# Optimization experiments

Measured on AMD Instinct MI355X. Metric: run time of the kernel, lower is better.

Reference implementation:

```python
import jax, jax.numpy as jnp
import numpy as np

B, N, DIM = 16, 577, 768
HEADS, HEAD_DIM = 12, 64
QKV_DIM = HEADS * HEAD_DIM
MAX_REL = 14
TABLE_ROWS = 2 * MAX_REL + 2  # 30


def _rel_indices(n, max_rel):
    # Static (shape-only) 2D relative-position index matrices with CLS padding.
    m = n - 1
    side = int(m ** 0.5)
    r = np.arange(m)
    dv = r[None, :] // side - r[:, None] // side
    dh = r[None, :] % side - r[:, None] % side
    iv = np.clip(dv, -max_rel, max_rel) + max_rel + 1
    ih = np.clip(dh, -max_rel, max_rel) + max_rel + 1
    iv = np.pad(iv, ((1, 0), (1, 0)))  # CLS row/col -> index 0
    ih = np.pad(ih, ((1, 0), (1, 0)))
    return jnp.asarray(iv), jnp.asarray(ih)


def setup_inputs() -> dict:
    key = jax.random.key(0)
    ks = jax.random.split(key, 8)
    return {
        "x": jax.random.normal(ks[0], (B, N, DIM), jnp.float32),
        "qkv_w": jax.random.normal(ks[1], (3 * QKV_DIM, DIM), jnp.float32) * 0.02,
        "proj_w": jax.random.normal(ks[2], (DIM, QKV_DIM), jnp.float32) * 0.02,
        "proj_b": jnp.zeros((DIM,), jnp.float32),
        "tab_kv": jax.random.normal(ks[3], (TABLE_ROWS, HEAD_DIM), jnp.float32) * 0.02,
        "tab_kh": jax.random.normal(ks[4], (TABLE_ROWS, HEAD_DIM), jnp.float32) * 0.02,
        "tab_vv": jax.random.normal(ks[5], (TABLE_ROWS, HEAD_DIM), jnp.float32) * 0.02,
        "tab_vh": jax.random.normal(ks[6], (TABLE_ROWS, HEAD_DIM), jnp.float32) * 0.02,
    }


def reference(x, qkv_w, proj_w, proj_b, tab_kv, tab_kh, tab_vv, tab_vh):
    b, n, _ = x.shape
    scale = HEAD_DIM ** -0.5
    # qkv: [b,n,3*qkv_dim] -> [3,b,h,n,d]
    qkv = (x @ qkv_w.T).reshape(b, n, 3, HEADS, HEAD_DIM).transpose(2, 0, 3, 1, 4)
    q, k, v = qkv[0], qkv[1], qkv[2]
    attn = jnp.einsum('bhqd,bhkd->bhqk', q, k) * scale
    iv, ih = _rel_indices(n, MAX_REL)
    r_p_k = tab_kv[iv] + tab_kh[ih]  # [n,n,d]
    attn = attn + jnp.einsum('bhqd,qkd->bhqk', q, r_p_k) * scale
    attn = jax.nn.softmax(attn, axis=-1)
    out = jnp.einsum('bhqk,bhkd->bhqd', attn, v)
    r_p_v = tab_vv[iv] + tab_vh[ih]  # [n,n,d]
    out = out + jnp.einsum('bhqk,qkd->bhqd', attn, r_p_v)
    out = out.transpose(0, 2, 1, 3).reshape(b, n, QKV_DIM)
    return out @ proj_w.T + proj_b
```

## Files before the change

kernel.cpp:

```cpp
#include <hip/hip_runtime.h>


#define BB    16
#define NNq   577
#define DIMM  768
#define NHh   12
#define HD    64
#define MM    9232
#define QT    64
#define KT    64
#define NPAD  640
#define NW3   2304

typedef _Float16 h8 __attribute__((ext_vector_type(8)));
typedef _Float16 h4 __attribute__((ext_vector_type(4)));
typedef float    f4 __attribute__((ext_vector_type(4)));

__device__ inline h8 pack8(float4 a, float4 b) {
    h8 r;
    r[0]=(_Float16)a.x; r[1]=(_Float16)a.y; r[2]=(_Float16)a.z; r[3]=(_Float16)a.w;
    r[4]=(_Float16)b.x; r[5]=(_Float16)b.y; r[6]=(_Float16)b.z; r[7]=(_Float16)b.w;
    return r;
}

__global__ void init_all(const float* __restrict__ x, const float* __restrict__ w,
                         const float* __restrict__ pw,
                         _Float16* __restrict__ M2g, _Float16* __restrict__ vh,
                         _Float16* __restrict__ xh, _Float16* __restrict__ wh,
                         _Float16* __restrict__ pwh)
{
    const size_t id = (size_t)blockIdx.x*256 + threadIdx.x;
    if (id < NPAD*64) {
        const int key = (int)id >> 6, bin = (int)id & 63;
        int vb = 255, hb = 255;
        if (key == 0)      { vb = 24; hb = 49; }
        else if (key < NNq){ const int kq = key-1, kv = kq/24; vb = kv; hb = 25 + (kq - kv*24); }
        M2g[bin*NPAD + key] =
            ((key < NNq) && (bin==vb || bin==hb || bin==50)) ? (_Float16)1.f : (_Float16)0.f;
        return;
    }
    const size_t vid = id - NPAD*64;
    if (vid < (size_t)BB*NHh*HD*64) {
        const int head = (int)(vid >> 12);
        const int rem  = (int)vid & 4095;
        const int d    = rem >> 6;
        const int col  = 576 + (rem & 63);
        vh[(size_t)head*(HD*NPAD) + (size_t)d*NPAD + col] = (_Float16)0.f;
        return;
    }
    const size_t cid = vid - (size_t)BB*NHh*HD*64;
    const size_t NX = (size_t)MM*DIMM/4;
    const size_t NW = (size_t)NW3*DIMM/4;
    const size_t NP = (size_t)DIMM*DIMM/4;
    const float4* src; h4* dst; size_t j;
    if (cid < NX)            { src = (const float4*)x;  dst = (h4*)xh;  j = cid; }
    else if (cid < NX+NW)    { src = (const float4*)w;  dst = (h4*)wh;  j = cid - NX; }
    else if (cid < NX+NW+NP) { src = (const float4*)pw; dst = (h4*)pwh; j = cid - NX - NW; }
    else return;
    const float4 v = src[j];
    h4 hh; hh[0]=(_Float16)v.x; hh[1]=(_Float16)v.y; hh[2]=(_Float16)v.z; hh[3]=(_Float16)v.w;
    dst[j] = hh;
}

template <typename F>
__device__ __forceinline__ void gemm128f2(const _Float16* __restrict__ Ah_g,
                                          const _Float16* __restrict__ Bh_g,
                                          F epi)
{
    __shared__ _Float16 Ah[128][72], Bh[128][72];
    const int t  = threadIdx.x;
    const int wv = t >> 6, lane = t & 63, lo = lane & 15, g = lane >> 4;
    const int gb = g << 3;
    const int wm = (wv >> 1) << 6, wn = (wv & 1) << 6;
    const int bm = blockIdx.y << 7, bn = blockIdx.x << 7;
    f4 acc[4][4] = {};
    const int lr = t >> 1;
    const int lc = (t & 1) << 5;
    const int am = bm + lr;
    const bool aok = am < MM;
    const _Float16* arh = Ah_g + (size_t)(aok ? am : 0) * DIMM + lc;
    const _Float16* brh = Bh_g + (size_t)(bn + lr) * DIMM + lc;

    for (int k0 = 0; k0 < DIMM; k0 += 64) {
        h8 a0 = {}, a1 = {}, a2 = {}, a3 = {};
        if (aok) {
            a0 = *(const h8*)(arh + k0);      a1 = *(const h8*)(arh + k0 + 8);
            a2 = *(const h8*)(arh + k0 + 16); a3 = *(const h8*)(arh + k0 + 24);
        }
        const h8 b0 = *(const h8*)(brh + k0),      b1 = *(const h8*)(brh + k0 + 8);
        const h8 b2 = *(const h8*)(brh + k0 + 16), b3 = *(const h8*)(brh + k0 + 24);
        __syncthreads();
        *(h8*)&Ah[lr][lc]    = a0; *(h8*)&Ah[lr][lc+8]  = a1;
        *(h8*)&Ah[lr][lc+16] = a2; *(h8*)&Ah[lr][lc+24] = a3;
        *(h8*)&Bh[lr][lc]    = b0; *(h8*)&Bh[lr][lc+8]  = b1;
        *(h8*)&Bh[lr][lc+16] = b2; *(h8*)&Bh[lr][lc+24] = b3;
        __syncthreads();
        {
            h8 fah[4], fbh[4];
            #pragma unroll
            for (int i = 0; i < 4; ++i) {
                fah[i] = *(const h8*)&Ah[wm + 16*i + lo][gb];
                fbh[i] = *(const h8*)&Bh[wn + 16*i + lo][gb];
            }
            #pragma unroll
            for (int mi = 0; mi < 4; ++mi) {
                #pragma unroll
                for (int ni = 0; ni < 4; ++ni)
                    acc[mi][ni] = __builtin_amdgcn_mfma_f32_16x16x32_f16(fah[mi], fbh[ni], acc[mi][ni], 0, 0, 0);
            }
        }
        {
            h8 fah[4], fbh[4];
            #pragma unroll
            for (int i = 0; i < 4; ++i) {
                fah[i] = *(const h8*)&Ah[wm + 16*i + lo][32 + gb];
                fbh[i] = *(const h8*)&Bh[wn + 16*i + lo][32 + gb];
            }
            #pragma unroll
            for (int mi = 0; mi < 4; ++mi) {
                #pragma unroll
                for (int ni = 0; ni < 4; ++ni)
                    acc[mi][ni] = __builtin_amdgcn_mfma_f32_16x16x32_f16(fah[mi], fbh[ni], acc[mi][ni], 0, 0, 0);
            }
        }
    }
    epi(acc, bm, bn, wm, wn, lo, g);
}

__global__ __launch_bounds__(256, 3)
void qkv_gemm(const _Float16* __restrict__ xh, const _Float16* __restrict__ wh,
              _Float16* __restrict__ qh, _Float16* __restrict__ kh, _Float16* __restrict__ vh)
{
    gemm128f2(xh, wh, [=](f4 (&acc)[4][4], int bm, int bn, int wm, int wn, int lo, int g) {
        const int three = bn / 768;
        const int cb    = bn - three * 768;
        #pragma unroll
        for (int mi = 0; mi < 4; ++mi) {
            #pragma unroll
            for (int reg = 0; reg < 4; ++reg) {
                const int m = bm + wm + 16*mi + 4*g + reg;
                if (m >= MM) continue;
                const int b_ = m / NNq;
                const int n_ = m - b_ * NNq;
                #pragma unroll
                for (int ni = 0; ni < 4; ++ni) {
                    const int n  = cb + wn + 16*ni + lo;
                    const int hh = n >> 6;
                    const int d  = n & 63;
                    if (three == 0) {
                        qh[((size_t)(b_*NHh + hh)*NPAD + n_)*HD + d] =
                            (_Float16)(acc[mi][ni][reg] * 0.18033688f);
                    } else if (three == 1) {
                        kh[((size_t)(b_*NHh + hh)*NPAD + n_)*HD + d] = (_Float16)acc[mi][ni][reg];
                    } else {
                        vh[((size_t)(b_*NHh + hh)*HD + d)*NPAD + n_] = (_Float16)acc[mi][ni][reg];
                    }
                }
            }
        }
    });
}

__global__ __launch_bounds__(256, 3)
void proj_gemm(const _Float16* __restrict__ aoh, const _Float16* __restrict__ pwh,
               const float* __restrict__ bias, float* __restrict__ out)
{
    gemm128f2(aoh, pwh, [=](f4 (&acc)[4][4], int bm, int bn, int wm, int wn, int lo, int g) {
        #pragma unroll
        for (int ni = 0; ni < 4; ++ni) {
            const int n  = bn + wn + 16*ni + lo;
            const float bb = bias[n];
            #pragma unroll
            for (int mi = 0; mi < 4; ++mi) {
                #pragma unroll
                for (int reg = 0; reg < 4; ++reg) {
                    const int m = bm + wm + 16*mi + 4*g + reg;
                    if (m >= MM) continue;
                    out[(size_t)m*DIMM + n] = acc[mi][ni][reg] + bb;
                }
            }
        }
    });
}

__global__ __launch_bounds__(256, 2)
void attn_fused(const _Float16* __restrict__ qh,
                const _Float16* __restrict__ kh, const _Float16* __restrict__ vh,
                const float* __restrict__ tkv, const float* __restrict__ tkh,
                const float* __restrict__ tvv, const float* __restrict__ tvh,
                const _Float16* __restrict__ M2g,
                _Float16* __restrict__ aoh)
{
    __shared__ __align__(16) char smem[34048];
    _Float16 (*qrelS)[72] = (_Float16(*)[72])(smem);
    _Float16 (*Pt)[72]    = (_Float16(*)[72])(smem + 9216);
    float    (*TvS)[65]   = (float(*)[65])(smem + 18432);
    float    (*binsS)[52] = (float(*)[52])(smem);

    const int t    = threadIdx.x;
    const int w    = t >> 6;
    const int lane = t & 63;
    const int lo   = lane & 15;
    const int g    = lane >> 4;
    const int gb   = g << 3;

    const int blk = blockIdx.x;
    const int x8  = blk & 7;
    const int r_  = blk >> 3;
    const int hq  = r_ / 10;
    const int qt  = r_ - hq*10;
    const int bh  = x8 + (hq << 3);
    const int qt0 = qt * QT;
    const int qrow = 16*w + 4*g;
    const _Float16* qp = qh + (size_t)bh * (NPAD*HD);
    const _Float16* kp = kh + (size_t)bh * (NPAD*HD);
    const _Float16* vp = vh + (size_t)bh * (HD*NPAD);

    for (int e = t; e < 60*64; e += 256) {
        const int r = e >> 6, d = e & 63;
        TvS[r][d] = (r < 30) ? tvv[r*HD + d] : tvh[(r-30)*HD + d];
    }

    const h8 a0 = *(const h8*)(qp + (size_t)(qt0 + 16*w + lo)*HD + gb);
    const h8 a1 = *(const h8*)(qp + (size_t)(qt0 + 16*w + lo)*HD + 32 + gb);

    {
        f4 qacc[4] = {f4{0,0,0,0}, f4{0,0,0,0}, f4{0,0,0,0}, f4{0,0,0,0}};
        #pragma unroll
        for (int c = 0; c < 4; ++c) {
            const int r16 = 16*c + lo;
            const float* src = (r16 < 30) ? (tkv + r16*HD) : (tkh + (r16-30)*HD);
            h8 tb0 = {}, tb1 = {};
            if (r16 < 60) {
                tb0 = pack8(*(const float4*)(src + gb),      *(const float4*)(src + gb + 4));
                tb1 = pack8(*(const float4*)(src + 32 + gb), *(const float4*)(src + 32 + gb + 4));
            }
            qacc[c] = __builtin_amdgcn_mfma_f32_16x16x32_f16(a0, tb0, qacc[c], 0, 0, 0);
            qacc[c] = __builtin_amdgcn_mfma_f32_16x16x32_f16(a1, tb1, qacc[c], 0, 0, 0);
        }
        #pragma unroll
        for (int c = 0; c < 4; ++c) {
            #pragma unroll
            for (int i = 0; i < 4; ++i)
                qrelS[qrow + i][16*c + lo] = (_Float16)qacc[c][i];
        }
    }

    int qv_[4], qh_[4];
    bool q0_[4];
    #pragma unroll
    for (int i = 0; i < 4; ++i) {
        const int qgl = qt0 + qrow + i;
        q0_[i] = (qgl == 0);
        int qq = qgl - 1; if (qq < 0) qq = 0;
        qv_[i] = qq / 24;
        qh_[i] = qq - qv_[i]*24;
    }

    f4 o_acc [4] = {f4{0,0,0,0}, f4{0,0,0,0}, f4{0,0,0,0}, f4{0,0,0,0}};
    f4 binacc[4] = {f4{0,0,0,0}, f4{0,0,0,0}, f4{0,0,0,0}, f4{0,0,0,0}};

    for (int kt0 = 0; kt0 < 576; kt0 += KT) {
        h8 kb0[4], kb1[4], v0r[4], v1r[4], m20[4], m21[4];
        #pragma unroll
        for (int c = 0; c < 4; ++c) {
            const int key = kt0 + 16*c + lo;
            kb0[c] = *(const h8*)(kp + (size_t)key*HD + gb);
            kb1[c] = *(const h8*)(kp + (size_t)key*HD + 32 + gb);
            const int dd = 16*c + lo;
            v0r[c] = *(const h8*)(vp + (size_t)dd*NPAD + kt0 + gb);
            v1r[c] = *(const h8*)(vp + (size_t)dd*NPAD + kt0 + 32 + gb);
            m20[c] = *(const h8*)(M2g + (size_t)dd*NPAD + kt0 + gb);
            m21[c] = *(const h8*)(M2g + (size_t)dd*NPAD + kt0 + 32 + gb);
        }
        float srel[4][4];
        #pragma unroll
        for (int c = 0; c < 4; ++c) {
            const int key = kt0 + 16*c + lo;
            int kk = key - 1; if (kk < 0) kk = 0;
            const int kv  = kk / 24;
            const int kh2 = kk - kv*24;
            const bool kz = (key == 0);
            #pragma unroll
            for (int i = 0; i < 4; ++i) {
                int colv, colh;
                if (kz || q0_[i]) { colv = 0; colh = 30; }
                else {
                    int dv = kv  - qv_[i]; dv = min(14, max(-14, dv));
                    int dh = kh2 - qh_[i]; dh = min(14, max(-14, dh));
                    colv = dv + 15;
                    colh = 45 + dh;
                }
                srel[c][i] = (float)qrelS[qrow+i][colv] + (float)qrelS[qrow+i][colh];
            }
        }
        f4 Sc[4];
        #pragma unroll
        for (int c = 0; c < 4; ++c) {
            f4 acc = f4{0,0,0,0};
            acc = __builtin_amdgcn_mfma_f32_16x16x32_f16(a0, kb0[c], acc, 0, 0, 0);
            acc = __builtin_amdgcn_mfma_f32_16x16x32_f16(a1, kb1[c], acc, 0, 0, 0);
            Sc[c] = acc;
        }
        #pragma unroll
        for (int c = 0; c < 4; ++c) {
            #pragma unroll
            for (int i = 0; i < 4; ++i) {
                const float p = exp2f(Sc[c][i] + srel[c][i]);
                Pt[qrow+i][16*c + lo] = (_Float16)p;
            }
        }
        const h8 p0 = *(const h8*)&Pt[16*w + lo][gb];
        const h8 p1 = *(const h8*)&Pt[16*w + lo][32 + gb];
        #pragma unroll
        for (int c = 0; c < 4; ++c) {
            binacc[c] = __builtin_amdgcn_mfma_f32_16x16x32_f16(p0, m20[c], binacc[c], 0, 0, 0);
            binacc[c] = __builtin_amdgcn_mfma_f32_16x16x32_f16(p1, m21[c], binacc[c], 0, 0, 0);
        }
        #pragma unroll
        for (int c = 0; c < 4; ++c) {
            o_acc[c] = __builtin_amdgcn_mfma_f32_16x16x32_f16(p0, v0r[c], o_acc[c], 0, 0, 0);
            o_acc[c] = __builtin_amdgcn_mfma_f32_16x16x32_f16(p1, v1r[c], o_acc[c], 0, 0, 0);
        }
    }

    {
        const int kt0 = 576;
        h8 kb0_, kb1_, v0r[4], v1r[4], m20[4], m21[4];
        kb0_ = *(const h8*)(kp + (size_t)(kt0 + lo)*HD + gb);
        kb1_ = *(const h8*)(kp + (size_t)(kt0 + lo)*HD + 32 + gb);
        #pragma unroll
        for (int c = 0; c < 4; ++c) {
            const int dd = 16*c + lo;
            v0r[c] = *(const h8*)(vp + (size_t)dd*NPAD + kt0 + gb);
            v1r[c] = *(const h8*)(vp + (size_t)dd*NPAD + kt0 + 32 + gb);
            m20[c] = *(const h8*)(M2g + (size_t)dd*NPAD + kt0 + gb);
            m21[c] = *(const h8*)(M2g + (size_t)dd*NPAD + kt0 + 32 + gb);
        }
        float srel0[4];
        {
            const int key = kt0 + lo;
            int kk = key - 1; if (kk < 0) kk = 0;
            const int kv  = kk / 24;
            const int kh2 = kk - kv*24;
            #pragma unroll
            for (int i = 0; i < 4; ++i) {
                int colv, colh;
                if (q0_[i]) { colv = 0; colh = 30; }
                else {
                    int dv = kv  - qv_[i]; dv = min(14, max(-14, dv));
                    int dh = kh2 - qh_[i]; dh = min(14, max(-14, dh));
                    colv = dv + 15;
                    colh = 45 + dh;
                }
                srel0[i] = (float)qrelS[qrow+i][colv] + (float)qrelS[qrow+i][colh];
            }
        }
        f4 Sc0 = f4{0,0,0,0};
        Sc0 = __builtin_amdgcn_mfma_f32_16x16x32_f16(a0, kb0_, Sc0, 0, 0, 0);
        Sc0 = __builtin_amdgcn_mfma_f32_16x16x32_f16(a1, kb1_, Sc0, 0, 0, 0);
        {
            const bool ok = (kt0 + lo) < NNq;
            #pragma unroll
            for (int i = 0; i < 4; ++i) {
                const float p = ok ? exp2f(Sc0[i] + srel0[i]) : 0.f;
                Pt[qrow+i][lo] = (_Float16)p;
            }
            #pragma unroll
            for (int c = 1; c < 4; ++c) {
                #pragma unroll
                for (int i = 0; i < 4; ++i)
                    Pt[qrow+i][16*c + lo] = (_Float16)0.f;
            }
        }
        const h8 p0 = *(const h8*)&Pt[16*w + lo][gb];
        const h8 p1 = *(const h8*)&Pt[16*w + lo][32 + gb];
        #pragma unroll
        for (int c = 0; c < 4; ++c) {
            binacc[c] = __builtin_amdgcn_mfma_f32_16x16x32_f16(p0, m20[c], binacc[c], 0, 0, 0);
            binacc[c] = __builtin_amdgcn_mfma_f32_16x16x32_f16(p1, m21[c], binacc[c], 0, 0, 0);
        }
        #pragma unroll
        for (int c = 0; c < 4; ++c) {
            o_acc[c] = __builtin_amdgcn_mfma_f32_16x16x32_f16(p0, v0r[c], o_acc[c], 0, 0, 0);
            o_acc[c] = __builtin_amdgcn_mfma_f32_16x16x32_f16(p1, v1r[c], o_acc[c], 0, 0, 0);
        }
    }

    __syncthreads();
    #pragma unroll
    for (int c = 0; c < 4; ++c) {
        const int bc = 16*c + lo;
        if (bc <= 50) {
            #pragma unroll
            for (int i = 0; i < 4; ++i) binsS[qrow+i][bc] = binacc[c][i];
        }
    }
    __syncthreads();

    const int b_ = bh / NHh;
    const int h_ = bh - b_*NHh;
    #pragma unroll
    for (int i = 0; i < 4; ++i) {
        const int qr  = qrow + i;
        const int qgl = qt0 + qr;
        if (qgl >= NNq) continue;
        const float l    = binsS[qr][50];
        const float invl = 1.f / l;
        float o[4] = {o_acc[0][i], o_acc[1][i], o_acc[2][i], o_acc[3][i]};
        if (qgl == 0) {
            #pragma unroll
            for (int c = 0; c < 4; ++c) {
                const int d = 16*c + lo;
                o[c] += l * (TvS[0][d] + TvS[30][d]);
            }
        } else {
            #pragma unroll
            for (int bin = 0; bin < 24; ++bin) {
                const float wq = binsS[qr][bin];
                int dv = bin - qv_[i]; dv = min(14, max(-14, dv));
                #pragma unroll
                for (int c = 0; c < 4; ++c) o[c] += wq * TvS[dv+15][16*c + lo];
            }
            {
                const float wq = binsS[qr][24];
                #pragma unroll
                for (int c = 0; c < 4; ++c) o[c] += wq * TvS[0][16*c + lo];
            }
            #pragma unroll
            for (int bin = 0; bin < 24; ++bin) {
                const float wq = binsS[qr][25+bin];
                int dh = bin - qh_[i]; dh = min(14, max(-14, dh));
                #pragma unroll
                for (int c = 0; c < 4; ++c) o[c] += wq * TvS[45+dh][16*c + lo];
            }
            {
                const float wq = binsS[qr][49];
                #pragma unroll
                for (int c = 0; c < 4; ++c) o[c] += wq * TvS[30][16*c + lo];
            }
        }
        _Float16* dst = aoh + (size_t)(b_*NNq + qgl)*DIMM + h_*HD;
        #pragma unroll
        for (int c = 0; c < 4; ++c) dst[16*c + lo] = (_Float16)(o[c] * invl);
    }
}

extern "C" void kernel_launch(void* const* d_in, const int* in_sizes, int n_in,
                              void* d_out, int out_size, void* d_ws, size_t ws_size,
                              hipStream_t stream)
{
    const float* x      = (const float*)d_in[0];
    const float* qkv_w  = (const float*)d_in[1];
    const float* proj_w = (const float*)d_in[2];
    const float* proj_b = (const float*)d_in[3];
    const float* tkv    = (const float*)d_in[4];
    const float* tkh    = (const float*)d_in[5];
    const float* tvv    = (const float*)d_in[6];
    const float* tvh    = (const float*)d_in[7];
    float* out = (float*)d_out;
    float* ws  = (float*)d_ws;

    const size_t KV = (size_t)BB * NHh * NPAD * HD;
    _Float16* qh  = (_Float16*)ws;
    _Float16* kh  = qh + KV;
    _Float16* vh  = kh + KV;
    _Float16* aoh = vh + KV;
    _Float16* M2g = aoh + (size_t)MM*DIMM;
    _Float16* xh  = M2g + NPAD*64;
    _Float16* wh  = xh + (size_t)MM*DIMM;
    _Float16* pwh = wh + (size_t)NW3*DIMM;

    dim3 b256(256, 1, 1);
    init_all<<<12460, b256, 0, stream>>>(x, qkv_w, proj_w, M2g, vh, xh, wh, pwh);

    dim3 g1(NW3/128, (MM + 127)/128, 1);
    qkv_gemm<<<g1, b256, 0, stream>>>(xh, wh, qh, kh, vh);

    attn_fused<<<dim3(1920,1,1), b256, 0, stream>>>(qh, kh, vh, tkv, tkh, tvv, tvh, M2g, aoh);

    dim3 g3(DIMM/128, (MM + 127)/128, 1);
    proj_gemm<<<g3, b256, 0, stream>>>(aoh, pwh, proj_b, out);
}
```

Before: 433.0 us.

## Process two 64-row query tiles per attention block to reuse K/V/M2 loads

Each attention workgroup now handles 128 query rows as two 64-row sub-tiles, so every K, V and M2 fragment loaded from global memory feeds twice the MFMA work. The grid is halved to 960 blocks and shared memory grows to hold the doubled qrel, P and bins buffers. The cost is more accumulator registers and LDS per block, which may lower occupancy under the 2-blocks-per-SIMD launch bound. The last tile also computes rows past 577 that are then discarded.

```diff
diff --git a/kernel.cpp b/kernel.cpp
--- a/kernel.cpp
+++ b/kernel.cpp
@@ -7,7 +7,6 @@
 #define NHh   12
 #define HD    64
 #define MM    9232
-#define QT    64
 #define KT    64
 #define NPAD  640
 #define NW3   2304
@@ -191,10 +190,10 @@
                 const _Float16* __restrict__ M2g,
                 _Float16* __restrict__ aoh)
 {
-    __shared__ __align__(16) char smem[34048];
+    __shared__ __align__(16) char smem[52464];
     _Float16 (*qrelS)[72] = (_Float16(*)[72])(smem);
-    _Float16 (*Pt)[72]    = (_Float16(*)[72])(smem + 9216);
-    float    (*TvS)[65]   = (float(*)[65])(smem + 18432);
+    _Float16 (*Pt)[72]    = (_Float16(*)[72])(smem + 18432);
+    float    (*TvS)[65]   = (float(*)[65])(smem + 36864);
     float    (*binsS)[52] = (float(*)[52])(smem);
 
     const int t    = threadIdx.x;
@@ -207,10 +206,10 @@
     const int blk = blockIdx.x;
     const int x8  = blk & 7;
     const int r_  = blk >> 3;
-    const int hq  = r_ / 10;
-    const int qt  = r_ - hq*10;
+    const int hq  = r_ / 5;
+    const int qt  = r_ - hq*5;
     const int bh  = x8 + (hq << 3);
-    const int qt0 = qt * QT;
+    const int qt0 = qt * 128;
     const int qrow = 16*w + 4*g;
     const _Float16* qp = qh + (size_t)bh * (NPAD*HD);
     const _Float16* kp = kh + (size_t)bh * (NPAD*HD);
@@ -221,11 +220,14 @@
         TvS[r][d] = (r < 30) ? tvv[r*HD + d] : tvh[(r-30)*HD + d];
     }
 
-    const h8 a0 = *(const h8*)(qp + (size_t)(qt0 + 16*w + lo)*HD + gb);
-    const h8 a1 = *(const h8*)(qp + (size_t)(qt0 + 16*w + lo)*HD + 32 + gb);
+    const h8 a0A = *(const h8*)(qp + (size_t)(qt0 +      16*w + lo)*HD + gb);
+    const h8 a1A = *(const h8*)(qp + (size_t)(qt0 +      16*w + lo)*HD + 32 + gb);
+    const h8 a0B = *(const h8*)(qp + (size_t)(qt0 + 64 + 16*w + lo)*HD + gb);
+    const h8 a1B = *(const h8*)(qp + (size_t)(qt0 + 64 + 16*w + lo)*HD + 32 + gb);
 
     {
-        f4 qacc[4] = {f4{0,0,0,0}, f4{0,0,0,0}, f4{0,0,0,0}, f4{0,0,0,0}};
+        f4 qaccA[4] = {f4{0,0,0,0}, f4{0,0,0,0}, f4{0,0,0,0}, f4{0,0,0,0}};
+        f4 qaccB[4] = {f4{0,0,0,0}, f4{0,0,0,0}, f4{0,0,0,0}, f4{0,0,0,0}};
         #pragma unroll
         for (int c = 0; c < 4; ++c) {
             const int r16 = 16*c + lo;
@@ -235,30 +237,39 @@
                 tb0 = pack8(*(const float4*)(src + gb),      *(const float4*)(src + gb + 4));
                 tb1 = pack8(*(const float4*)(src + 32 + gb), *(const float4*)(src + 32 + gb + 4));
             }
-            qacc[c] = __builtin_amdgcn_mfma_f32_16x16x32_f16(a0, tb0, qacc[c], 0, 0, 0);
-            qacc[c] = __builtin_amdgcn_mfma_f32_16x16x32_f16(a1, tb1, qacc[c], 0, 0, 0);
-        }
-        #pragma unroll
-        for (int c = 0; c < 4; ++c) {
-            #pragma unroll
-            for (int i = 0; i < 4; ++i)
-                qrelS[qrow + i][16*c + lo] = (_Float16)qacc[c][i];
-        }
-    }
-
-    int qv_[4], qh_[4];
-    bool q0_[4];
+            qaccA[c] = __builtin_amdgcn_mfma_f32_16x16x32_f16(a0A, tb0, qaccA[c], 0, 0, 0);
+            qaccA[c] = __builtin_amdgcn_mfma_f32_16x16x32_f16(a1A, tb1, qaccA[c], 0, 0, 0);
+            qaccB[c] = __builtin_amdgcn_mfma_f32_16x16x32_f16(a0B, tb0, qaccB[c], 0, 0, 0);
+            qaccB[c] = __builtin_amdgcn_mfma_f32_16x16x32_f16(a1B, tb1, qaccB[c], 0, 0, 0);
+        }
+        #pragma unroll
+        for (int c = 0; c < 4; ++c) {
+            #pragma unroll
+            for (int i = 0; i < 4; ++i) {
+                qrelS[qrow + i][16*c + lo]      = (_Float16)qaccA[c][i];
+                qrelS[64 + qrow + i][16*c + lo] = (_Float16)qaccB[c][i];
+            }
+        }
+    }
+
+    int qv_[2][4], qh_[2][4];
+    bool q0_[2][4];
     #pragma unroll
-    for (int i = 0; i < 4; ++i) {
-        const int qgl = qt0 + qrow + i;
-        q0_[i] = (qgl == 0);
-        int qq = qgl - 1; if (qq < 0) qq = 0;
-        qv_[i] = qq / 24;
-        qh_[i] = qq - qv_[i]*24;
-    }
-
-    f4 o_acc [4] = {f4{0,0,0,0}, f4{0,0,0,0}, f4{0,0,0,0}, f4{0,0,0,0}};
-    f4 binacc[4] = {f4{0,0,0,0}, f4{0,0,0,0}, f4{0,0,0,0}, f4{0,0,0,0}};
+    for (int tb = 0; tb < 2; ++tb) {
+        #pragma unroll
+        for (int i = 0; i < 4; ++i) {
+            const int qgl = qt0 + 64*tb + qrow + i;
+            q0_[tb][i] = (qgl == 0);
+            int qq = qgl - 1; if (qq < 0) qq = 0;
+            qv_[tb][i] = qq / 24;
+            qh_[tb][i] = qq - qv_[tb][i]*24;
+        }
+    }
+
+    f4 o_accA [4] = {f4{0,0,0,0}, f4{0,0,0,0}, f4{0,0,0,0}, f4{0,0,0,0}};
+    f4 binaccA[4] = {f4{0,0,0,0}, f4{0,0,0,0}, f4{0,0,0,0}, f4{0,0,0,0}};
+    f4 o_accB [4] = {f4{0,0,0,0}, f4{0,0,0,0}, f4{0,0,0,0}, f4{0,0,0,0}};
+    f4 binaccB[4] = {f4{0,0,0,0}, f4{0,0,0,0}, f4{0,0,0,0}, f4{0,0,0,0}};
 
     for (int kt0 = 0; kt0 < 576; kt0 += KT) {
         h8 kb0[4], kb1[4], v0r[4], v1r[4], m20[4], m21[4];
@@ -273,54 +284,95 @@
             m20[c] = *(const h8*)(M2g + (size_t)dd*NPAD + kt0 + gb);
             m21[c] = *(const h8*)(M2g + (size_t)dd*NPAD + kt0 + 32 + gb);
         }
-        float srel[4][4];
+        int kvc[4], khc[4];
+        bool kzc[4];
         #pragma unroll
         for (int c = 0; c < 4; ++c) {
             const int key = kt0 + 16*c + lo;
             int kk = key - 1; if (kk < 0) kk = 0;
-            const int kv  = kk / 24;
-            const int kh2 = kk - kv*24;
-            const bool kz = (key == 0);
-            #pragma unroll
-            for (int i = 0; i < 4; ++i) {
-                int colv, colh;
-                if (kz || q0_[i]) { colv = 0; colh = 30; }
-                else {
-                    int dv = kv  - qv_[i]; dv = min(14, max(-14, dv));
-                    int dh = kh2 - qh_[i]; dh = min(14, max(-14, dh));
-                    colv = dv + 15;
-                    colh = 45 + dh;
-                }
-                srel[c][i] = (float)qrelS[qrow+i][colv] + (float)qrelS[qrow+i][colh];
-            }
-        }
-        f4 Sc[4];
-        #pragma unroll
-        for (int c = 0; c < 4; ++c) {
-            f4 acc = f4{0,0,0,0};
-            acc = __builtin_amdgcn_mfma_f32_16x16x32_f16(a0, kb0[c], acc, 0, 0, 0);
-            acc = __builtin_amdgcn_mfma_f32_16x16x32_f16(a1, kb1[c], acc, 0, 0, 0);
-            Sc[c] = acc;
-        }
-        #pragma unroll
-        for (int c = 0; c < 4; ++c) {
-            #pragma unroll
-            for (int i = 0; i < 4; ++i) {
-                const float p = exp2f(Sc[c][i] + srel[c][i]);
-                Pt[qrow+i][16*c + lo] = (_Float16)p;
-            }
-        }
-        const h8 p0 = *(const h8*)&Pt[16*w + lo][gb];
-        const h8 p1 = *(const h8*)&Pt[16*w + lo][32 + gb];
-        #pragma unroll
-        for (int c = 0; c < 4; ++c) {
-            binacc[c] = __builtin_amdgcn_mfma_f32_16x16x32_f16(p0, m20[c], binacc[c], 0, 0, 0);
-            binacc[c] = __builtin_amdgcn_mfma_f32_16x16x32_f16(p1, m21[c], binacc[c], 0, 0, 0);
-        }
-        #pragma unroll
-        for (int c = 0; c < 4; ++c) {
-            o_acc[c] = __builtin_amdgcn_mfma_f32_16x16x32_f16(p0, v0r[c], o_acc[c], 0, 0, 0);
-            o_acc[c] = __builtin_amdgcn_mfma_f32_16x16x32_f16(p1, v1r[c], o_acc[c], 0, 0, 0);
+            kvc[c] = kk / 24;
+            khc[c] = kk - kvc[c]*24;
+            kzc[c] = (key == 0);
+        }
+        {
+            float srel[4][4];
+            #pragma unroll
+            for (int c = 0; c < 4; ++c) {
+                #pragma unroll
+                for (int i = 0; i < 4; ++i) {
+                    int colv, colh;
+                    if (kzc[c] || q0_[0][i]) { colv = 0; colh = 30; }
+                    else {
+                        int dv = kvc[c] - qv_[0][i]; dv = min(14, max(-14, dv));
+                        int dh = khc[c] - qh_[0][i]; dh = min(14, max(-14, dh));
+                        colv = dv + 15; colh = 45 + dh;
+                    }
+                    srel[c][i] = (float)qrelS[qrow+i][colv] + (float)qrelS[qrow+i][colh];
+                }
+            }
+            f4 Sc[4];
+            #pragma unroll
+            for (int c = 0; c < 4; ++c) {
+                f4 acc = f4{0,0,0,0};
+                acc = __builtin_amdgcn_mfma_f32_16x16x32_f16(a0A, kb0[c], acc, 0, 0, 0);
+                acc = __builtin_amdgcn_mfma_f32_16x16x32_f16(a1A, kb1[c], acc, 0, 0, 0);
+                Sc[c] = acc;
+            }
+            #pragma unroll
+            for (int c = 0; c < 4; ++c) {
+                #pragma unroll
+                for (int i = 0; i < 4; ++i)
+                    Pt[qrow+i][16*c + lo] = (_Float16)exp2f(Sc[c][i] + srel[c][i]);
+            }
+        }
+        {
+            float srel[4][4];
+            #pragma unroll
+            for (int c = 0; c < 4; ++c) {
+                #pragma unroll
+                for (int i = 0; i < 4; ++i) {
+                    int colv, colh;
+                    if (kzc[c] || q0_[1][i]) { colv = 0; colh = 30; }
+                    else {
+                        int dv = kvc[c] - qv_[1][i]; dv = min(14, max(-14, dv));
+                        int dh = khc[c] - qh_[1][i]; dh = min(14, max(-14, dh));
+                        colv = dv + 15; colh = 45 + dh;
+                    }
+                    srel[c][i] = (float)qrelS[64+qrow+i][colv] + (float)qrelS[64+qrow+i][colh];
+                }
+            }
+            f4 Sc[4];
+            #pragma unroll
+            for (int c = 0; c < 4; ++c) {
+                f4 acc = f4{0,0,0,0};
+                acc = __builtin_amdgcn_mfma_f32_16x16x32_f16(a0B, kb0[c], acc, 0, 0, 0);
+                acc = __builtin_amdgcn_mfma_f32_16x16x32_f16(a1B, kb1[c], acc, 0, 0, 0);
+                Sc[c] = acc;
+            }
+            #pragma unroll
+            for (int c = 0; c < 4; ++c) {
+                #pragma unroll
+                for (int i = 0; i < 4; ++i)
+                    Pt[64+qrow+i][16*c + lo] = (_Float16)exp2f(Sc[c][i] + srel[c][i]);
+            }
+        }
+        const h8 p0A = *(const h8*)&Pt[16*w + lo][gb];
+        const h8 p1A = *(const h8*)&Pt[16*w + lo][32 + gb];
+        const h8 p0B = *(const h8*)&Pt[64 + 16*w + lo][gb];
+        const h8 p1B = *(const h8*)&Pt[64 + 16*w + lo][32 + gb];
+        #pragma unroll
+        for (int c = 0; c < 4; ++c) {
+            binaccA[c] = __builtin_amdgcn_mfma_f32_16x16x32_f16(p0A, m20[c], binaccA[c], 0, 0, 0);
+            binaccA[c] = __builtin_amdgcn_mfma_f32_16x16x32_f16(p1A, m21[c], binaccA[c], 0, 0, 0);
+            binaccB[c] = __builtin_amdgcn_mfma_f32_16x16x32_f16(p0B, m20[c], binaccB[c], 0, 0, 0);
+            binaccB[c] = __builtin_amdgcn_mfma_f32_16x16x32_f16(p1B, m21[c], binaccB[c], 0, 0, 0);
+        }
+        #pragma unroll
+        for (int c = 0; c < 4; ++c) {
+            o_accA[c] = __builtin_amdgcn_mfma_f32_16x16x32_f16(p0A, v0r[c], o_accA[c], 0, 0, 0);
+            o_accA[c] = __builtin_amdgcn_mfma_f32_16x16x32_f16(p1A, v1r[c], o_accA[c], 0, 0, 0);
+            o_accB[c] = __builtin_amdgcn_mfma_f32_16x16x32_f16(p0B, v0r[c], o_accB[c], 0, 0, 0);
+            o_accB[c] = __builtin_amdgcn_mfma_f32_16x16x32_f16(p1B, v1r[c], o_accB[c], 0, 0, 0);
         }
     }
 
@@ -337,53 +389,76 @@
             m20[c] = *(const h8*)(M2g + (size_t)dd*NPAD + kt0 + gb);
             m21[c] = *(const h8*)(M2g + (size_t)dd*NPAD + kt0 + 32 + gb);
         }
-        float srel0[4];
+        const int key = kt0 + lo;
+        int kk = key - 1;
+        const int kv  = kk / 24;
+        const int kh2 = kk - kv*24;
+        const bool ok = key < NNq;
         {
-            const int key = kt0 + lo;
-            int kk = key - 1; if (kk < 0) kk = 0;
-            const int kv  = kk / 24;
-            const int kh2 = kk - kv*24;
+            float srel0[4];
             #pragma unroll
             for (int i = 0; i < 4; ++i) {
                 int colv, colh;
-                if (q0_[i]) { colv = 0; colh = 30; }
+                if (q0_[0][i]) { colv = 0; colh = 30; }
                 else {
-                    int dv = kv  - qv_[i]; dv = min(14, max(-14, dv));
-                    int dh = kh2 - qh_[i]; dh = min(14, max(-14, dh));
-                    colv = dv + 15;
-                    colh = 45 + dh;
+                    int dv = kv  - qv_[0][i]; dv = min(14, max(-14, dv));
+                    int dh = kh2 - qh_[0][i]; dh = min(14, max(-14, dh));
+                    colv = dv + 15; colh = 45 + dh;
                 }
                 srel0[i] = (float)qrelS[qrow+i][colv] + (float)qrelS[qrow+i][colh];
             }
-        }
-        f4 Sc0 = f4{0,0,0,0};
-        Sc0 = __builtin_amdgcn_mfma_f32_16x16x32_f16(a0, kb0_, Sc0, 0, 0, 0);
-        Sc0 = __builtin_amdgcn_mfma_f32_16x16x32_f16(a1, kb1_, Sc0, 0, 0, 0);
+            f4 Sc0 = f4{0,0,0,0};
+            Sc0 = __builtin_amdgcn_mfma_f32_16x16x32_f16(a0A, kb0_, Sc0, 0, 0, 0);
+            Sc0 = __builtin_amdgcn_mfma_f32_16x16x32_f16(a1A, kb1_, Sc0, 0, 0, 0);
+            #pragma unroll
+            for (int i = 0; i < 4; ++i)
+                Pt[qrow+i][lo] = (_Float16)(ok ? exp2f(Sc0[i] + srel0[i]) : 0.f);
+            #pragma unroll
+            for (int c = 1; c < 4; ++c)
+                #pragma unroll
+                for (int i = 0; i < 4; ++i) Pt[qrow+i][16*c + lo] = (_Float16)0.f;
+        }
         {
-            const bool ok = (kt0 + lo) < NNq;
+            float srel0[4];
             #pragma unroll
             for (int i = 0; i < 4; ++i) {
-                const float p = ok ? exp2f(Sc0[i] + srel0[i]) : 0.f;
-                Pt[qrow+i][lo] = (_Float16)p;
-            }
-            #pragma unroll
-            for (int c = 1; c < 4; ++c) {
-                #pragma unroll
-                for (int i = 0; i < 4; ++i)
-                    Pt[qrow+i][16*c + lo] = (_Float16)0.f;
-            }
-        }
-        const h8 p0 = *(const h8*)&Pt[16*w + lo][gb];
-        const h8 p1 = *(const h8*)&Pt[16*w + lo][32 + gb];
-        #pragma unroll
-        for (int c = 0; c < 4; ++c) {
-            binacc[c] = __builtin_amdgcn_mfma_f32_16x16x32_f16(p0, m20[c], binacc[c], 0, 0, 0);
-            binacc[c] = __builtin_amdgcn_mfma_f32_16x16x32_f16(p1, m21[c], binacc[c], 0, 0, 0);
-        }
-        #pragma unroll
-        for (int c = 0; c < 4; ++c) {
-            o_acc[c] = __builtin_amdgcn_mfma_f32_16x16x32_f16(p0, v0r[c], o_acc[c], 0, 0, 0);
-            o_acc[c] = __builtin_amdgcn_mfma_f32_16x16x32_f16(p1, v1r[c], o_acc[c], 0, 0, 0);
+                int colv, colh;
+                if (q0_[1][i]) { colv = 0; colh = 30; }
+                else {
+                    int dv = kv  - qv_[1][i]; dv = min(14, max(-14, dv));
+                    int dh = kh2 - qh_[1][i]; dh = min(14, max(-14, dh));
+                    colv = dv + 15; colh = 45 + dh;
+                }
+                srel0[i] = (float)qrelS[64+qrow+i][colv] + (float)qrelS[64+qrow+i][colh];
+            }
+            f4 Sc0 = f4{0,0,0,0};
+            Sc0 = __builtin_amdgcn_mfma_f32_16x16x32_f16(a0B, kb0_, Sc0, 0, 0, 0);
+            Sc0 = __builtin_amdgcn_mfma_f32_16x16x32_f16(a1B, kb1_, Sc0, 0, 0, 0);
+            #pragma unroll
+            for (int i = 0; i < 4; ++i)
+                Pt[64+qrow+i][lo] = (_Float16)(ok ? exp2f(Sc0[i] + srel0[i]) : 0.f);
+            #pragma unroll
+            for (int c = 1; c < 4; ++c)
+                #pragma unroll
+                for (int i = 0; i < 4; ++i) Pt[64+qrow+i][16*c + lo] = (_Float16)0.f;
+        }
+        const h8 p0A = *(const h8*)&Pt[16*w + lo][gb];
+        const h8 p1A = *(const h8*)&Pt[16*w + lo][32 + gb];
+        const h8 p0B = *(const h8*)&Pt[64 + 16*w + lo][gb];
+        const h8 p1B = *(const h8*)&Pt[64 + 16*w + lo][32 + gb];
+        #pragma unroll
+        for (int c = 0; c < 4; ++c) {
+            binaccA[c] = __builtin_amdgcn_mfma_f32_16x16x32_f16(p0A, m20[c], binaccA[c], 0, 0, 0);
+            binaccA[c] = __builtin_amdgcn_mfma_f32_16x16x32_f16(p1A, m21[c], binaccA[c], 0, 0, 0);
+            binaccB[c] = __builtin_amdgcn_mfma_f32_16x16x32_f16(p0B, m20[c], binaccB[c], 0, 0, 0);
+            binaccB[c] = __builtin_amdgcn_mfma_f32_16x16x32_f16(p1B, m21[c], binaccB[c], 0, 0, 0);
+        }
+        #pragma unroll
+        for (int c = 0; c < 4; ++c) {
+            o_accA[c] = __builtin_amdgcn_mfma_f32_16x16x32_f16(p0A, v0r[c], o_accA[c], 0, 0, 0);
+            o_accA[c] = __builtin_amdgcn_mfma_f32_16x16x32_f16(p1A, v1r[c], o_accA[c], 0, 0, 0);
+            o_accB[c] = __builtin_amdgcn_mfma_f32_16x16x32_f16(p0B, v0r[c], o_accB[c], 0, 0, 0);
+            o_accB[c] = __builtin_amdgcn_mfma_f32_16x16x32_f16(p1B, v1r[c], o_accB[c], 0, 0, 0);
         }
     }
 
@@ -393,7 +468,10 @@
         const int bc = 16*c + lo;
         if (bc <= 50) {
             #pragma unroll
-            for (int i = 0; i < 4; ++i) binsS[qrow+i][bc] = binacc[c][i];
+            for (int i = 0; i < 4; ++i) {
+                binsS[qrow+i][bc]      = binaccA[c][i];
+                binsS[64+qrow+i][bc]   = binaccB[c][i];
+            }
         }
     }
     __syncthreads();
@@ -401,48 +479,52 @@
     const int b_ = bh / NHh;
     const int h_ = bh - b_*NHh;
     #pragma unroll
-    for (int i = 0; i < 4; ++i) {
-        const int qr  = qrow + i;
-        const int qgl = qt0 + qr;
-        if (qgl >= NNq) continue;
-        const float l    = binsS[qr][50];
-        const float invl = 1.f / l;
-        float o[4] = {o_acc[0][i], o_acc[1][i], o_acc[2][i], o_acc[3][i]};
-        if (qgl == 0) {
-            #pragma unroll
-            for (int c = 0; c < 4; ++c) {
-                const int d = 16*c + lo;
-                o[c] += l * (TvS[0][d] + TvS[30][d]);
-            }
-        } else {
-            #pragma unroll
-            for (int bin = 0; bin < 24; ++bin) {
-                const float wq = binsS[qr][bin];
-                int dv = bin - qv_[i]; dv = min(14, max(-14, dv));
-                #pragma unroll
-                for (int c = 0; c < 4; ++c) o[c] += wq * TvS[dv+15][16*c + lo];
-            }
-            {
-                const float wq = binsS[qr][24];
-                #pragma unroll
-                for (int c = 0; c < 4; ++c) o[c] += wq * TvS[0][16*c + lo];
-            }
-            #pragma unroll
-            for (int bin = 0; bin < 24; ++bin) {
-                const float wq = binsS[qr][25+bin];
-                int dh = bin - qh_[i]; dh = min(14, max(-14, dh));
-                #pragma unroll
-                for (int c = 0; c < 4; ++c) o[c] += wq * TvS[45+dh][16*c + lo];
-            }
-            {
-                const float wq = binsS[qr][49];
-                #pragma unroll
-                for (int c = 0; c < 4; ++c) o[c] += wq * TvS[30][16*c + lo];
-            }
-        }
-        _Float16* dst = aoh + (size_t)(b_*NNq + qgl)*DIMM + h_*HD;
-        #pragma unroll
-        for (int c = 0; c < 4; ++c) dst[16*c + lo] = (_Float16)(o[c] * invl);
+    for (int tb = 0; tb < 2; ++tb) {
+        #pragma unroll
+        for (int i = 0; i < 4; ++i) {
+            const int qr  = 64*tb + qrow + i;
+            const int qgl = qt0 + qr;
+            if (qgl >= NNq) continue;
+            const float l    = binsS[qr][50];
+            const float invl = 1.f / l;
+            const f4* oa = tb ? o_accB : o_accA;
+            float o[4] = {oa[0][i], oa[1][i], oa[2][i], oa[3][i]};
+            if (qgl == 0) {
+                #pragma unroll
+                for (int c = 0; c < 4; ++c) {
+                    const int d = 16*c + lo;
+                    o[c] += l * (TvS[0][d] + TvS[30][d]);
+                }
+            } else {
+                #pragma unroll
+                for (int bin = 0; bin < 24; ++bin) {
+                    const float wq = binsS[qr][bin];
+                    int dv = bin - qv_[tb][i]; dv = min(14, max(-14, dv));
+                    #pragma unroll
+                    for (int c = 0; c < 4; ++c) o[c] += wq * TvS[dv+15][16*c + lo];
+                }
+                {
+                    const float wq = binsS[qr][24];
+                    #pragma unroll
+                    for (int c = 0; c < 4; ++c) o[c] += wq * TvS[0][16*c + lo];
+                }
+                #pragma unroll
+                for (int bin = 0; bin < 24; ++bin) {
+                    const float wq = binsS[qr][25+bin];
+                    int dh = bin - qh_[tb][i]; dh = min(14, max(-14, dh));
+                    #pragma unroll
+                    for (int c = 0; c < 4; ++c) o[c] += wq * TvS[45+dh][16*c + lo];
+                }
+                {
+                    const float wq = binsS[qr][49];
+                    #pragma unroll
+                    for (int c = 0; c < 4; ++c) o[c] += wq * TvS[30][16*c + lo];
+                }
+            }
+            _Float16* dst = aoh + (size_t)(b_*NNq + qgl)*DIMM + h_*HD;
+            #pragma unroll
+            for (int c = 0; c < 4; ++c) dst[16*c + lo] = (_Float16)(o[c] * invl);
+        }
     }
 }
 
@@ -477,7 +559,7 @@
     dim3 g1(NW3/128, (MM + 127)/128, 1);
     qkv_gemm<<<g1, b256, 0, stream>>>(xh, wh, qh, kh, vh);
 
-    attn_fused<<<dim3(1920,1,1), b256, 0, stream>>>(qh, kh, vh, tkv, tkh, tvv, tvh, M2g, aoh);
+    attn_fused<<<dim3(960,1,1), b256, 0, stream>>>(qh, kh, vh, tkv, tkh, tvv, tvh, M2g, aoh);
 
     dim3 g3(DIMM/128, (MM + 127)/128, 1);
     proj_gemm<<<g3, b256, 0, stream>>>(aoh, pwh, proj_b, out);
```

Result: slower. 449.8 us (+3.9%).
